# Kernel optimization log

Measured on AMD Instinct MI355X. Metric: run time of the kernel, lower is better.

## Reference

```python
import math
import jax, jax.numpy as jnp
import numpy as np

N = 100000
E_RAND = 800000
IN_F, HID, OUT_F, HEADS = 128, 64, 64, 4
NOISE_SCALE = 1.0 * math.sqrt(2.0 * math.log(1.25 / 0.05))  # dp_rate=1, eps=1, del=0.05


def setup_inputs() -> dict:
    key = jax.random.key(0)
    ks = jax.random.split(key, 12)
    x = jax.random.normal(ks[0], (N, IN_F), dtype=jnp.float32)
    src_r = jax.random.randint(ks[1], (E_RAND,), 0, N, dtype=jnp.int32)
    dst_r = jax.random.randint(ks[2], (E_RAND,), 0, N, dtype=jnp.int32)
    loops = jnp.arange(N, dtype=jnp.int32)  # add_self_loop
    src = jnp.concatenate([src_r, loops])
    dst = jnp.concatenate([dst_r, loops])
    # layer 0: GATConv(in=128, out=64, heads=4)
    s0 = 1.0 / math.sqrt(IN_F)
    W0 = jax.random.normal(ks[3], (IN_F, HEADS * HID), dtype=jnp.float32) * s0
    al0 = jax.random.normal(ks[4], (HEADS, HID), dtype=jnp.float32) * 0.1
    ar0 = jax.random.normal(ks[5], (HEADS, HID), dtype=jnp.float32) * 0.1
    b0 = jnp.zeros((HEADS * HID,), dtype=jnp.float32)
    # layer 1: GATConv(in=256, out=64, heads=1)
    s1 = 1.0 / math.sqrt(HEADS * HID)
    W1 = jax.random.normal(ks[6], (HEADS * HID, OUT_F), dtype=jnp.float32) * s1
    al1 = jax.random.normal(ks[7], (1, OUT_F), dtype=jnp.float32) * 0.1
    ar1 = jax.random.normal(ks[8], (1, OUT_F), dtype=jnp.float32) * 0.1
    b1 = jnp.zeros((OUT_F,), dtype=jnp.float32)
    # DP gaussian noise added after first GAT layer (torch.normal(0,1,x.shape))
    noise = jax.random.normal(ks[9], (N, HEADS * HID), dtype=jnp.float32)
    return {"x": x, "src": src, "dst": dst, "W0": W0, "al0": al0, "ar0": ar0,
            "b0": b0, "W1": W1, "al1": al1, "ar1": ar1, "b1": b1, "noise": noise}


def gat_conv(x, src, dst, W, al, ar, b, apply_act):
    """DGL GATConv: per-edge attention, edge softmax over dst, scatter-sum."""
    H, D = al.shape
    h = (x @ W).reshape(-1, H, D)                      # [N,H,D]
    el = jnp.sum(h * al, axis=-1)                      # [N,H]
    er = jnp.sum(h * ar, axis=-1)                      # [N,H]
    e = jax.nn.leaky_relu(el[src] + er[dst], 0.2)      # [E,H]
    emax = jax.ops.segment_max(e, dst, num_segments=N) # [N,H]
    a = jnp.exp(e - emax[dst])
    denom = jax.ops.segment_sum(a, dst, num_segments=N)
    alpha = a / denom[dst]                             # [E,H] edge softmax
    msg = h[src] * alpha[:, :, None]                   # [E,H,D]
    out = jax.ops.segment_sum(msg, dst, num_segments=N) + b.reshape(1, H, D)
    if apply_act:
        out = jax.nn.leaky_relu(out, 0.01)             # F.leaky_relu default slope
    return out.reshape(-1, H * D)                      # flatten(1)


def reference(x, src, dst, W0, al0, ar0, b0, W1, al1, ar1, b1, noise):
    h = gat_conv(x, src, dst, W0, al0, ar0, b0, apply_act=True)   # [N, 256]
    h = h + NOISE_SCALE * noise                                   # DP noise after layer 0
    out = gat_conv(h, src, dst, W1, al1, ar1, b1, apply_act=False)  # [N, 64]
    return out
```

## Files before the change

### kernel.cpp

```cpp
#include <hip/hip_runtime.h>
#include <hip/hip_bf16.h>
#include <math.h>

#define IN_F 128
#define HID 64
#define HEADS 4
#define HD0 (HEADS * HID)
#define OUT_F 64
#define NOISE_SCALE 2.5372725354060904f

typedef __bf16 bf16x8 __attribute__((ext_vector_type(8)));
typedef float f32x4 __attribute__((ext_vector_type(4)));

__device__ __forceinline__ float bf2f(unsigned short u) {
    return __uint_as_float(((unsigned)u) << 16);
}
__device__ __forceinline__ unsigned short f2bf(float f) {
    unsigned u = __float_as_uint(f);
    u = u + 0x7fffu + ((u >> 16) & 1u);
    return (unsigned short)(u >> 16);
}

__global__ __launch_bounds__(256) void tcast_kernel(
    const float* __restrict__ W, unsigned short* __restrict__ Wt, int K, int NC) {
    int i = blockIdx.x * 256 + threadIdx.x;
    if (i >= K * NC) return;
    int n = i / K, k = i % K;
    Wt[n * K + k] = f2bf(W[(size_t)k * NC + n]);
}

template <int K, bool CASTA, int H>
__global__ __launch_bounds__(256) void gemm_fused_kernel(
    const void* __restrict__ Av, const unsigned short* __restrict__ Bt,
    unsigned short* __restrict__ C, const float* __restrict__ al,
    const float* __restrict__ ar, float* __restrict__ el,
    float* __restrict__ er, int M, int NC) {
    constexpr int BSTR = K + 8;
    constexpr int ASTR = 40;
    __shared__ __align__(16) unsigned short Bs[64 * BSTR];
    __shared__ __align__(16) unsigned short As[128 * ASTR];
    const int tid = threadIdx.x;
    const int lane = tid & 63, w = tid >> 6;
    const int row0 = blockIdx.y * 128;
    const int n0 = blockIdx.x * 64;
    for (int i = tid; i < 64 * (K / 8); i += 256) {
        int n = i / (K / 8), kc = i % (K / 8);
        *(uint4*)(Bs + n * BSTR + kc * 8) =
            *(const uint4*)(Bt + (size_t)(n0 + n) * K + kc * 8);
    }
    f32x4 acc[2][4] = {};
    const int q = lane >> 4, c = lane & 15;
    const int r_st = tid >> 1, hh = tid & 1;
    for (int k0 = 0; k0 < K; k0 += 32) {
        int gr = row0 + r_st;
        uint4 av0 = make_uint4(0, 0, 0, 0), av1 = make_uint4(0, 0, 0, 0);
        if (gr < M) {
            if (CASTA) {
                const float* A = (const float*)Av;
                const float* ap = A + (size_t)gr * K + k0 + hh * 16;
                float4 f0 = *(const float4*)(ap);
                float4 f1 = *(const float4*)(ap + 4);
                float4 f2 = *(const float4*)(ap + 8);
                float4 f3 = *(const float4*)(ap + 12);
                ushort4 u0, u1, u2, u3;
                u0.x = f2bf(f0.x); u0.y = f2bf(f0.y); u0.z = f2bf(f0.z); u0.w = f2bf(f0.w);
                u1.x = f2bf(f1.x); u1.y = f2bf(f1.y); u1.z = f2bf(f1.z); u1.w = f2bf(f1.w);
                u2.x = f2bf(f2.x); u2.y = f2bf(f2.y); u2.z = f2bf(f2.z); u2.w = f2bf(f2.w);
                u3.x = f2bf(f3.x); u3.y = f2bf(f3.y); u3.z = f2bf(f3.z); u3.w = f2bf(f3.w);
                av0 = make_uint4(((unsigned)u0.y << 16) | u0.x, ((unsigned)u0.w << 16) | u0.z,
                                 ((unsigned)u1.y << 16) | u1.x, ((unsigned)u1.w << 16) | u1.z);
                av1 = make_uint4(((unsigned)u2.y << 16) | u2.x, ((unsigned)u2.w << 16) | u2.z,
                                 ((unsigned)u3.y << 16) | u3.x, ((unsigned)u3.w << 16) | u3.z);
            } else {
                const unsigned short* A = (const unsigned short*)Av;
                const unsigned short* ap = A + (size_t)gr * K + k0 + hh * 16;
                av0 = *(const uint4*)(ap);
                av1 = *(const uint4*)(ap + 8);
            }
        }
        __syncthreads();
        *(uint4*)(As + r_st * ASTR + hh * 16) = av0;
        *(uint4*)(As + r_st * ASTR + hh * 16 + 8) = av1;
        __syncthreads();
        bf16x8 af[2], bfr[4];
        af[0] = *(const bf16x8*)(As + (w * 32 + c) * ASTR + q * 8);
        af[1] = *(const bf16x8*)(As + (w * 32 + 16 + c) * ASTR + q * 8);
#pragma unroll
        for (int nt = 0; nt < 4; ++nt)
            bfr[nt] = *(const bf16x8*)(Bs + (nt * 16 + c) * BSTR + k0 + q * 8);
#pragma unroll
        for (int mt = 0; mt < 2; ++mt)
#pragma unroll
            for (int nt = 0; nt < 4; ++nt)
                acc[mt][nt] = __builtin_amdgcn_mfma_f32_16x16x32_bf16(
                    af[mt], bfr[nt], acc[mt][nt], 0, 0, 0);
    }
    float alv[4], arv[4];
#pragma unroll
    for (int nt = 0; nt < 4; ++nt) {
        alv[nt] = al[n0 + nt * 16 + c];
        arv[nt] = ar[n0 + nt * 16 + c];
    }
    const int head = n0 >> 6;
#pragma unroll
    for (int mt = 0; mt < 2; ++mt) {
#pragma unroll
        for (int r = 0; r < 4; ++r) {
            int grow = row0 + w * 32 + mt * 16 + q * 4 + r;
            bool ok = grow < M;
            float elp = 0.f, erp = 0.f;
#pragma unroll
            for (int nt = 0; nt < 4; ++nt) {
                float v = acc[mt][nt][r];
                elp += v * alv[nt];
                erp += v * arv[nt];
                if (ok) C[(size_t)grow * NC + n0 + nt * 16 + c] = f2bf(v);
            }
#pragma unroll
            for (int o = 8; o > 0; o >>= 1) {
                elp += __shfl_down(elp, o, 16);
                erp += __shfl_down(erp, o, 16);
            }
            if (c == 0 && ok) {
                el[(size_t)grow * H + head] = elp;
                er[(size_t)grow * H + head] = erp;
            }
        }
    }
}

__global__ __launch_bounds__(256) void degree_kernel(
    const int* __restrict__ dst, int* __restrict__ deg, int E) {
    int e = blockIdx.x * 256 + threadIdx.x;
    if (e < E) atomicAdd(&deg[dst[e]], 1);
}

__global__ __launch_bounds__(256) void scan_block_kernel(
    const int* __restrict__ deg, int* __restrict__ off,
    int* __restrict__ bsum, int N) {
    __shared__ int s[256];
    int i = blockIdx.x * 256 + threadIdx.x;
    int v = (i < N) ? deg[i] : 0;
    s[threadIdx.x] = v;
    __syncthreads();
    for (int d = 1; d < 256; d <<= 1) {
        int t = (threadIdx.x >= d) ? s[threadIdx.x - d] : 0;
        __syncthreads();
        s[threadIdx.x] += t;
        __syncthreads();
    }
    if (i < N) off[i] = s[threadIdx.x] - v;
    if (threadIdx.x == 255) bsum[blockIdx.x] = s[255];
}

__global__ __launch_bounds__(512) void scan_partials_kernel(int* __restrict__ bsum, int nb) {
    __shared__ int s[512];
    int v = (threadIdx.x < nb) ? bsum[threadIdx.x] : 0;
    s[threadIdx.x] = v;
    __syncthreads();
    for (int d = 1; d < 512; d <<= 1) {
        int t = (threadIdx.x >= d) ? s[threadIdx.x - d] : 0;
        __syncthreads();
        s[threadIdx.x] += t;
        __syncthreads();
    }
    if (threadIdx.x < nb) bsum[threadIdx.x] = s[threadIdx.x] - v;
}

__global__ __launch_bounds__(256) void add_offsets_kernel(
    int* __restrict__ off, const int* __restrict__ bsum, int N, int E) {
    int i = blockIdx.x * 256 + threadIdx.x;
    if (i < N) off[i] += bsum[blockIdx.x];
    if (i == 0) off[N] = E;
}

__global__ __launch_bounds__(256) void fill_csr_kernel(
    const int* __restrict__ src, const int* __restrict__ dst,
    int* __restrict__ cur, int* __restrict__ csr_src, int E) {
    int e = blockIdx.x * 256 + threadIdx.x;
    if (e >= E) return;
    int d = dst[e];
    int pos = atomicAdd(&cur[d], 1);
    csr_src[pos] = src[e];
}

template <int H>
__global__ __launch_bounds__(256) void alpha_kernel(
    const int* __restrict__ off, const int* __restrict__ csr_src,
    const float* __restrict__ el, const float* __restrict__ er,
    float* __restrict__ alpha, float* __restrict__ rden, int N) {
    int t = blockIdx.x * 256 + threadIdx.x;
    int n = t / H, hd = t % H;
    if (n >= N) return;
    float ern = er[(size_t)n * H + hd];
    int beg = off[n], end = off[n + 1];
    float m = -INFINITY;
    for (int p = beg; p < end; ++p) {
        float e = el[(size_t)csr_src[p] * H + hd] + ern;
        e = e > 0.f ? e : 0.2f * e;
        m = fmaxf(m, e);
    }
    float l = 0.f;
    for (int p = beg; p < end; ++p) {
        float e = el[(size_t)csr_src[p] * H + hd] + ern;
        e = e > 0.f ? e : 0.2f * e;
        float wv = __expf(e - m);
        alpha[(size_t)p * H + hd] = wv;
        l += wv;
    }
    rden[(size_t)n * H + hd] = 1.f / l;
}

__global__ __launch_bounds__(256) void agg0_kernel(
    const int* __restrict__ off, const int* __restrict__ csr_src,
    const unsigned short* __restrict__ h,
    const float* __restrict__ alpha,
    const float* __restrict__ rden,
    const float* __restrict__ b0, const float* __restrict__ noise,
    unsigned short* __restrict__ out, int N) {
    int gt = blockIdx.x * 256 + threadIdx.x;
    int n = gt >> 6;
    int lane = gt & 63;
    if (n >= N) return;
    int hd = lane >> 4;
    int beg = off[n], end = off[n + 1];
    float ax = 0.f, ay = 0.f, az = 0.f, aw = 0.f;
    int p = beg;
    for (; p + 2 <= end; p += 2) {
        int s0 = csr_src[p], s1 = csr_src[p + 1];
        float w0 = alpha[(size_t)p * 4 + hd];
        float w1 = alpha[(size_t)(p + 1) * 4 + hd];
        ushort4 u0 = *(const ushort4*)(h + (size_t)s0 * HD0 + lane * 4);
        ushort4 u1 = *(const ushort4*)(h + (size_t)s1 * HD0 + lane * 4);
        ax += w0 * bf2f(u0.x) + w1 * bf2f(u1.x);
        ay += w0 * bf2f(u0.y) + w1 * bf2f(u1.y);
        az += w0 * bf2f(u0.z) + w1 * bf2f(u1.z);
        aw += w0 * bf2f(u0.w) + w1 * bf2f(u1.w);
    }
    if (p < end) {
        int s0 = csr_src[p];
        float w0 = alpha[(size_t)p * 4 + hd];
        ushort4 u0 = *(const ushort4*)(h + (size_t)s0 * HD0 + lane * 4);
        ax += w0 * bf2f(u0.x);
        ay += w0 * bf2f(u0.y);
        az += w0 * bf2f(u0.z);
        aw += w0 * bf2f(u0.w);
    }
    float rd = rden[(size_t)n * 4 + hd];
    const float4 bv = *(const float4*)(b0 + lane * 4);
    const float4 nv = *(const float4*)(noise + (size_t)n * HD0 + lane * 4);
    float ox = ax * rd + bv.x; ox = ox > 0.f ? ox : 0.01f * ox; ox += NOISE_SCALE * nv.x;
    float oy = ay * rd + bv.y; oy = oy > 0.f ? oy : 0.01f * oy; oy += NOISE_SCALE * nv.y;
    float oz = az * rd + bv.z; oz = oz > 0.f ? oz : 0.01f * oz; oz += NOISE_SCALE * nv.z;
    float ow = aw * rd + bv.w; ow = ow > 0.f ? ow : 0.01f * ow; ow += NOISE_SCALE * nv.w;
    ushort4 o;
    o.x = f2bf(ox); o.y = f2bf(oy); o.z = f2bf(oz); o.w = f2bf(ow);
    *(ushort4*)(out + (size_t)n * HD0 + lane * 4) = o;
}

__global__ __launch_bounds__(256) void agg1_kernel(
    const int* __restrict__ off, const int* __restrict__ csr_src,
    const unsigned short* __restrict__ h,
    const float* __restrict__ alpha,
    const float* __restrict__ rden,
    const float* __restrict__ b1, float* __restrict__ out, int N) {
    int gt = blockIdx.x * 256 + threadIdx.x;
    int n = gt >> 6;
    int lane = gt & 63;
    if (n >= N) return;
    int beg = off[n], end = off[n + 1];
    float acc = 0.f;
    int p = beg;
    for (; p + 4 <= end; p += 4) {
        int s0 = csr_src[p], s1 = csr_src[p + 1], s2 = csr_src[p + 2], s3 = csr_src[p + 3];
        float w0 = alpha[p], w1 = alpha[p + 1], w2 = alpha[p + 2], w3 = alpha[p + 3];
        float v0 = bf2f(h[(size_t)s0 * 64 + lane]);
        float v1 = bf2f(h[(size_t)s1 * 64 + lane]);
        float v2 = bf2f(h[(size_t)s2 * 64 + lane]);
        float v3 = bf2f(h[(size_t)s3 * 64 + lane]);
        acc += w0 * v0 + w1 * v1 + w2 * v2 + w3 * v3;
    }
    for (; p < end; ++p) {
        acc += alpha[p] * bf2f(h[(size_t)csr_src[p] * 64 + lane]);
    }
    out[(size_t)n * 64 + lane] = acc * rden[n] + b1[lane];
}

extern "C" void kernel_launch(void* const* d_in, const int* in_sizes, int n_in,
                              void* d_out, int out_size, void* d_ws, size_t ws_size,
                              hipStream_t stream) {
    const float* x     = (const float*)d_in[0];
    const int*   src   = (const int*)d_in[1];
    const int*   dst   = (const int*)d_in[2];
    const float* W0    = (const float*)d_in[3];
    const float* al0   = (const float*)d_in[4];
    const float* ar0   = (const float*)d_in[5];
    const float* b0    = (const float*)d_in[6];
    const float* W1    = (const float*)d_in[7];
    const float* al1   = (const float*)d_in[8];
    const float* ar1   = (const float*)d_in[9];
    const float* b1    = (const float*)d_in[10];
    const float* noise = (const float*)d_in[11];

    const int N = in_sizes[0] / IN_F;
    const int E = in_sizes[1];
    const int NB = (N + 255) / 256;

    char* p = (char*)d_ws;
    unsigned short* h0     = (unsigned short*)p; p += (size_t)N * HD0 * 2;
    unsigned short* agg0b  = (unsigned short*)p; p += (size_t)N * HD0 * 2;
    unsigned short* h1     = (unsigned short*)p; p += (size_t)N * OUT_F * 2;
    unsigned short* W0t    = (unsigned short*)p; p += (size_t)IN_F * HD0 * 2;
    unsigned short* W1t    = (unsigned short*)p; p += (size_t)HD0 * OUT_F * 2;
    float* el     = (float*)p; p += (size_t)N * HEADS * 4;
    float* er     = (float*)p; p += (size_t)N * HEADS * 4;
    float* alpha0 = (float*)p; p += (size_t)E * HEADS * 4;
    float* rden0  = (float*)p; p += (size_t)N * HEADS * 4;
    float* alpha1 = (float*)p; p += (size_t)E * 4;
    float* rden1  = (float*)p; p += (size_t)N * 4;
    int* deg    = (int*)p; p += (size_t)N * 4;
    int* cur    = (int*)p; p += (size_t)N * 4;
    int* off    = (int*)p; p += ((size_t)N + 4) * 4;
    int* bsum   = (int*)p; p += 512 * 4;
    int* csr_src= (int*)p; p += (size_t)E * 4;

    tcast_kernel<<<(IN_F * HD0 + 255) / 256, 256, 0, stream>>>(W0, W0t, IN_F, HD0);
    tcast_kernel<<<(HD0 * OUT_F + 255) / 256, 256, 0, stream>>>(W1, W1t, HD0, OUT_F);

    hipMemsetAsync(deg, 0, (size_t)N * sizeof(int), stream);
    degree_kernel<<<(E + 255) / 256, 256, 0, stream>>>(dst, deg, E);
    scan_block_kernel<<<NB, 256, 0, stream>>>(deg, off, bsum, N);
    scan_partials_kernel<<<1, 512, 0, stream>>>(bsum, NB);
    add_offsets_kernel<<<NB, 256, 0, stream>>>(off, bsum, N, E);
    hipMemcpyAsync(cur, off, (size_t)N * sizeof(int), hipMemcpyDeviceToDevice, stream);
    fill_csr_kernel<<<(E + 255) / 256, 256, 0, stream>>>(src, dst, cur, csr_src, E);

    const int MB = (N + 127) / 128;

    {
        dim3 grid(HD0 / 64, MB);
        gemm_fused_kernel<IN_F, true, HEADS><<<grid, 256, 0, stream>>>(
            x, W0t, h0, al0, ar0, el, er, N, HD0);
    }
    alpha_kernel<HEADS><<<(N * HEADS + 255) / 256, 256, 0, stream>>>(
        off, csr_src, el, er, alpha0, rden0, N);
    agg0_kernel<<<(N * 64 + 255) / 256, 256, 0, stream>>>(
        off, csr_src, h0, alpha0, rden0, b0, noise, agg0b, N);

    {
        dim3 grid(OUT_F / 64, MB);
        gemm_fused_kernel<HD0, false, 1><<<grid, 256, 0, stream>>>(
            agg0b, W1t, h1, al1, ar1, el, er, N, OUT_F);
    }
    alpha_kernel<1><<<(N + 255) / 256, 256, 0, stream>>>(
        off, csr_src, el, er, alpha1, rden1, N);
    agg1_kernel<<<(N * 64 + 255) / 256, 256, 0, stream>>>(
        off, csr_src, h1, alpha1, rden1, b1, (float*)d_out, N);
}
```

Baseline: 526.2 us.

## Fuse edge softmax into aggregation kernels and drop max subtraction

Removes the separate alpha kernels and computes the edge attention weights inline inside each aggregation kernel, accumulating the softmax denominator alongside the weighted sum. This avoids writing and re-reading per-edge alpha arrays and two kernel launches, and skips the max-subtraction pass. The trade-off is recomputing exp for each lane (16 or 64 times per edge), plus a risk of overflow if logits grow large, since the softmax is no longer max-stabilised. agg1 also drops from 4-way to 2-way unrolling.

```diff
diff --git a/kernel.cpp b/kernel.cpp
--- a/kernel.cpp
+++ b/kernel.cpp
@@ -184,38 +184,11 @@
     csr_src[pos] = src[e];
 }
 
-template <int H>
-__global__ __launch_bounds__(256) void alpha_kernel(
-    const int* __restrict__ off, const int* __restrict__ csr_src,
-    const float* __restrict__ el, const float* __restrict__ er,
-    float* __restrict__ alpha, float* __restrict__ rden, int N) {
-    int t = blockIdx.x * 256 + threadIdx.x;
-    int n = t / H, hd = t % H;
-    if (n >= N) return;
-    float ern = er[(size_t)n * H + hd];
-    int beg = off[n], end = off[n + 1];
-    float m = -INFINITY;
-    for (int p = beg; p < end; ++p) {
-        float e = el[(size_t)csr_src[p] * H + hd] + ern;
-        e = e > 0.f ? e : 0.2f * e;
-        m = fmaxf(m, e);
-    }
-    float l = 0.f;
-    for (int p = beg; p < end; ++p) {
-        float e = el[(size_t)csr_src[p] * H + hd] + ern;
-        e = e > 0.f ? e : 0.2f * e;
-        float wv = __expf(e - m);
-        alpha[(size_t)p * H + hd] = wv;
-        l += wv;
-    }
-    rden[(size_t)n * H + hd] = 1.f / l;
-}
-
 __global__ __launch_bounds__(256) void agg0_kernel(
     const int* __restrict__ off, const int* __restrict__ csr_src,
     const unsigned short* __restrict__ h,
-    const float* __restrict__ alpha,
-    const float* __restrict__ rden,
+    const float* __restrict__ el,
+    const float* __restrict__ er,
     const float* __restrict__ b0, const float* __restrict__ noise,
     unsigned short* __restrict__ out, int N) {
     int gt = blockIdx.x * 256 + threadIdx.x;
@@ -223,30 +196,38 @@
     int lane = gt & 63;
     if (n >= N) return;
     int hd = lane >> 4;
+    float ern = er[(size_t)n * 4 + hd];
     int beg = off[n], end = off[n + 1];
-    float ax = 0.f, ay = 0.f, az = 0.f, aw = 0.f;
+    float ax = 0.f, ay = 0.f, az = 0.f, aw = 0.f, l = 0.f;
     int p = beg;
     for (; p + 2 <= end; p += 2) {
         int s0 = csr_src[p], s1 = csr_src[p + 1];
-        float w0 = alpha[(size_t)p * 4 + hd];
-        float w1 = alpha[(size_t)(p + 1) * 4 + hd];
+        float e0 = el[(size_t)s0 * 4 + hd] + ern;
+        float e1 = el[(size_t)s1 * 4 + hd] + ern;
+        e0 = e0 > 0.f ? e0 : 0.2f * e0;
+        e1 = e1 > 0.f ? e1 : 0.2f * e1;
+        float w0 = __expf(e0), w1 = __expf(e1);
         ushort4 u0 = *(const ushort4*)(h + (size_t)s0 * HD0 + lane * 4);
         ushort4 u1 = *(const ushort4*)(h + (size_t)s1 * HD0 + lane * 4);
         ax += w0 * bf2f(u0.x) + w1 * bf2f(u1.x);
         ay += w0 * bf2f(u0.y) + w1 * bf2f(u1.y);
         az += w0 * bf2f(u0.z) + w1 * bf2f(u1.z);
         aw += w0 * bf2f(u0.w) + w1 * bf2f(u1.w);
+        l += w0 + w1;
     }
     if (p < end) {
         int s0 = csr_src[p];
-        float w0 = alpha[(size_t)p * 4 + hd];
+        float e0 = el[(size_t)s0 * 4 + hd] + ern;
+        e0 = e0 > 0.f ? e0 : 0.2f * e0;
+        float w0 = __expf(e0);
         ushort4 u0 = *(const ushort4*)(h + (size_t)s0 * HD0 + lane * 4);
         ax += w0 * bf2f(u0.x);
         ay += w0 * bf2f(u0.y);
         az += w0 * bf2f(u0.z);
         aw += w0 * bf2f(u0.w);
-    }
-    float rd = rden[(size_t)n * 4 + hd];
+        l += w0;
+    }
+    float rd = 1.f / l;
     const float4 bv = *(const float4*)(b0 + lane * 4);
     const float4 nv = *(const float4*)(noise + (size_t)n * HD0 + lane * 4);
     float ox = ax * rd + bv.x; ox = ox > 0.f ? ox : 0.01f * ox; ox += NOISE_SCALE * nv.x;
@@ -261,29 +242,37 @@
 __global__ __launch_bounds__(256) void agg1_kernel(
     const int* __restrict__ off, const int* __restrict__ csr_src,
     const unsigned short* __restrict__ h,
-    const float* __restrict__ alpha,
-    const float* __restrict__ rden,
+    const float* __restrict__ el,
+    const float* __restrict__ er,
     const float* __restrict__ b1, float* __restrict__ out, int N) {
     int gt = blockIdx.x * 256 + threadIdx.x;
     int n = gt >> 6;
     int lane = gt & 63;
     if (n >= N) return;
+    float ern = er[n];
     int beg = off[n], end = off[n + 1];
-    float acc = 0.f;
+    float acc = 0.f, l = 0.f;
     int p = beg;
-    for (; p + 4 <= end; p += 4) {
-        int s0 = csr_src[p], s1 = csr_src[p + 1], s2 = csr_src[p + 2], s3 = csr_src[p + 3];
-        float w0 = alpha[p], w1 = alpha[p + 1], w2 = alpha[p + 2], w3 = alpha[p + 3];
+    for (; p + 2 <= end; p += 2) {
+        int s0 = csr_src[p], s1 = csr_src[p + 1];
+        float e0 = el[s0] + ern, e1 = el[s1] + ern;
+        e0 = e0 > 0.f ? e0 : 0.2f * e0;
+        e1 = e1 > 0.f ? e1 : 0.2f * e1;
+        float w0 = __expf(e0), w1 = __expf(e1);
         float v0 = bf2f(h[(size_t)s0 * 64 + lane]);
         float v1 = bf2f(h[(size_t)s1 * 64 + lane]);
-        float v2 = bf2f(h[(size_t)s2 * 64 + lane]);
-        float v3 = bf2f(h[(size_t)s3 * 64 + lane]);
-        acc += w0 * v0 + w1 * v1 + w2 * v2 + w3 * v3;
-    }
-    for (; p < end; ++p) {
-        acc += alpha[p] * bf2f(h[(size_t)csr_src[p] * 64 + lane]);
-    }
-    out[(size_t)n * 64 + lane] = acc * rden[n] + b1[lane];
+        acc += w0 * v0 + w1 * v1;
+        l += w0 + w1;
+    }
+    if (p < end) {
+        int s0 = csr_src[p];
+        float e0 = el[s0] + ern;
+        e0 = e0 > 0.f ? e0 : 0.2f * e0;
+        float w0 = __expf(e0);
+        acc += w0 * bf2f(h[(size_t)s0 * 64 + lane]);
+        l += w0;
+    }
+    out[(size_t)n * 64 + lane] = acc / l + b1[lane];
 }
 
 extern "C" void kernel_launch(void* const* d_in, const int* in_sizes, int n_in,
@@ -314,10 +303,6 @@
     unsigned short* W1t    = (unsigned short*)p; p += (size_t)HD0 * OUT_F * 2;
     float* el     = (float*)p; p += (size_t)N * HEADS * 4;
     float* er     = (float*)p; p += (size_t)N * HEADS * 4;
-    float* alpha0 = (float*)p; p += (size_t)E * HEADS * 4;
-    float* rden0  = (float*)p; p += (size_t)N * HEADS * 4;
-    float* alpha1 = (float*)p; p += (size_t)E * 4;
-    float* rden1  = (float*)p; p += (size_t)N * 4;
     int* deg    = (int*)p; p += (size_t)N * 4;
     int* cur    = (int*)p; p += (size_t)N * 4;
     int* off    = (int*)p; p += ((size_t)N + 4) * 4;
@@ -342,18 +327,14 @@
         gemm_fused_kernel<IN_F, true, HEADS><<<grid, 256, 0, stream>>>(
             x, W0t, h0, al0, ar0, el, er, N, HD0);
     }
-    alpha_kernel<HEADS><<<(N * HEADS + 255) / 256, 256, 0, stream>>>(
-        off, csr_src, el, er, alpha0, rden0, N);
     agg0_kernel<<<(N * 64 + 255) / 256, 256, 0, stream>>>(
-        off, csr_src, h0, alpha0, rden0, b0, noise, agg0b, N);
+        off, csr_src, h0, el, er, b0, noise, agg0b, N);
 
     {
         dim3 grid(OUT_F / 64, MB);
         gemm_fused_kernel<HD0, false, 1><<<grid, 256, 0, stream>>>(
             agg0b, W1t, h1, al1, ar1, el, er, N, OUT_F);
     }
-    alpha_kernel<1><<<(N + 255) / 256, 256, 0, stream>>>(
-        off, csr_src, el, er, alpha1, rden1, N);
     agg1_kernel<<<(N * 64 + 255) / 256, 256, 0, stream>>>(
-        off, csr_src, h1, alpha1, rden1, b1, (float*)d_out, N);
-}
+        off, csr_src, h1, el, er, b1, (float*)d_out, N);
+}
```

New measurement: 502.5 us. 1.05x faster.
